# Kernel optimization log

Hardware: AMD Instinct MI355X
Metric: run time of the kernel (lower is better)

## Reference

```python
import jax, jax.numpy as jnp
import numpy as np
import math

NUM_HEADS = 16
DIM_EMB = 1024
DIM_HEAD = DIM_EMB // NUM_HEADS
BATCH = 2
SEQ = 2048


def setup_inputs() -> dict:
    key = jax.random.key(0)
    k_x, k_wq, k_bq, k_wo, k_bo = jax.random.split(key, 5)
    s_in = 1.0 / math.sqrt(DIM_EMB)
    return {
        "x": jax.random.normal(k_x, (BATCH, SEQ, DIM_EMB), dtype=jnp.float32),
        "W_qkv": jax.random.uniform(k_wq, (DIM_EMB, 3 * DIM_EMB), minval=-s_in, maxval=s_in, dtype=jnp.float32),
        "b_qkv": jax.random.uniform(k_bq, (3 * DIM_EMB,), minval=-s_in, maxval=s_in, dtype=jnp.float32),
        "W_out": jax.random.uniform(k_wo, (DIM_EMB, DIM_EMB), minval=-s_in, maxval=s_in, dtype=jnp.float32),
        "b_out": jax.random.uniform(k_bo, (DIM_EMB,), minval=-s_in, maxval=s_in, dtype=jnp.float32),
    }


def reference(x, W_qkv, b_qkv, W_out, b_out):
    B, L, E = x.shape
    H, Dh = NUM_HEADS, DIM_HEAD
    # QKV projection: (B, L, 3E)
    qkv = jnp.einsum("ble,ef->blf", x, W_qkv) + b_qkv
    # Faithful to the original's view: (B, L, 3E) -> (B, H, L, 3*Dh)
    qkv = qkv.reshape(B, H, L, 3 * Dh)
    q, k, v = jnp.split(qkv, 3, axis=-1)  # each (B, H, L, Dh)
    scale = 1.0 / math.sqrt(Dh)
    scores = jnp.einsum("bhqd,bhkd->bhqk", q, k) * scale  # (B, H, L, L)
    weights = jax.nn.softmax(scores, axis=-1)
    attn = jnp.einsum("bhqk,bhkd->bhqd", weights, v)  # (B, H, L, Dh)
    attn = attn.transpose(0, 2, 1, 3).reshape(B, L, E)
    return jnp.einsum("ble,ef->blf", attn, W_out) + b_out
```

## Files before the change

kernel.cpp:

```cpp
#include <hip/hip_runtime.h>
#include <math.h>

#define BATCH 2
#define SEQ   2048
#define EMB   1024
#define HEADS 16
#define N3E   3072
#define MROWS (BATCH*SEQ)

typedef __attribute__((ext_vector_type(8))) short  bf16x8;
typedef __attribute__((ext_vector_type(4))) float  f32x4;

__device__ __forceinline__ ushort f2bu(float f) {
    union { float f; unsigned u; } x; x.f = f;
    unsigned r = x.u + 0x7FFFu + ((x.u >> 16) & 1u);
    return (ushort)(r >> 16);
}

__global__ void cast_bf16(const float* __restrict__ in, ushort* __restrict__ out, int n4) {
    int i = blockIdx.x * blockDim.x + threadIdx.x;
    if (i < n4) {
        float4 v = ((const float4*)in)[i];
        ushort4 o;
        o.x = f2bu(v.x); o.y = f2bu(v.y); o.z = f2bu(v.z); o.w = f2bu(v.w);
        ((ushort4*)out)[i] = o;
    }
}

__global__ void transpose_cast(const float* __restrict__ W, ushort* __restrict__ Wt,
                               int K, int N) {
    __shared__ float t[32][33];
    const int bn = blockIdx.x * 32, bk = blockIdx.y * 32;
    const int tx = threadIdx.x, ty = threadIdx.y;
    #pragma unroll
    for (int j = 0; j < 4; ++j)
        t[ty + j * 8][tx] = W[(size_t)(bk + ty + j * 8) * N + bn + tx];
    __syncthreads();
    #pragma unroll
    for (int j = 0; j < 4; ++j)
        Wt[(size_t)(bn + ty + j * 8) * K + bk + tx] = f2bu(t[tx][ty + j * 8]);
}

__global__ void transpose_v(const ushort* __restrict__ qkv, ushort* __restrict__ VtG) {
    __shared__ ushort t[32][33];
    const int l0 = blockIdx.x * 32, d0 = blockIdx.y * 32, bh = blockIdx.z;
    const int rowbase = (bh >> 4) * SEQ + (bh & 15) * 128;
    const int tx = threadIdx.x, ty = threadIdx.y;
    #pragma unroll
    for (int j = 0; j < 4; ++j) {
        const int l = l0 + ty + j * 8;
        t[ty + j * 8][tx] = qkv[(size_t)(rowbase + (l >> 4)) * N3E
                                + (l & 15) * 192 + 128 + d0 + tx];
    }
    __syncthreads();
    #pragma unroll
    for (int j = 0; j < 4; ++j)
        VtG[((size_t)bh * 64 + d0 + ty + j * 8) * SEQ + l0 + tx] = t[tx][ty + j * 8];
}

template<bool OUT_BF16>
__global__ __launch_bounds__(256) void gemm_bt(const ushort* __restrict__ A,
                                               const ushort* __restrict__ Bt,
                                               const float* __restrict__ bias,
                                               void* __restrict__ Cout,
                                               int M, int N, int K)
{
    __shared__ ushort As[128][40];
    __shared__ ushort Bs[128][40];

    const int tid  = threadIdx.x;
    const int lane = tid & 63, w = tid >> 6;
    const int wr = w >> 1, wc = w & 1;
    const int l15 = lane & 15, l4 = lane >> 4;
    const int m0 = blockIdx.y * 128, n0 = blockIdx.x * 128;

    const f32x4 fzero = {0.f, 0.f, 0.f, 0.f};
    f32x4 acc[4][4];
    #pragma unroll
    for (int m = 0; m < 4; ++m)
        #pragma unroll
        for (int n = 0; n < 4; ++n) acc[m][n] = fzero;

    for (int k0 = 0; k0 < K; k0 += 32) {
        #pragma unroll
        for (int r = 0; r < 2; ++r) {
            const int i2 = tid + r * 256;
            const int row = i2 >> 2, seg = i2 & 3;
            *(bf16x8*)&As[row][seg * 8] =
                *(const bf16x8*)&A[(size_t)(m0 + row) * K + k0 + seg * 8];
            *(bf16x8*)&Bs[row][seg * 8] =
                *(const bf16x8*)&Bt[(size_t)(n0 + row) * K + k0 + seg * 8];
        }
        __syncthreads();

        bf16x8 am[4], bn[4];
        #pragma unroll
        for (int m = 0; m < 4; ++m) am[m] = *(bf16x8*)&As[wr * 64 + m * 16 + l15][l4 * 8];
        #pragma unroll
        for (int n = 0; n < 4; ++n) bn[n] = *(bf16x8*)&Bs[wc * 64 + n * 16 + l15][l4 * 8];
        #pragma unroll
        for (int m = 0; m < 4; ++m)
            #pragma unroll
            for (int n = 0; n < 4; ++n)
                acc[m][n] = __builtin_amdgcn_mfma_f32_16x16x32_bf16(am[m], bn[n], acc[m][n], 0, 0, 0);
        __syncthreads();
    }

    #pragma unroll
    for (int m = 0; m < 4; ++m)
        #pragma unroll
        for (int n = 0; n < 4; ++n)
            #pragma unroll
            for (int r = 0; r < 4; ++r) {
                const int row = m0 + wr * 64 + m * 16 + l4 * 4 + r;
                const int col = n0 + wc * 64 + n * 16 + l15;
                const float v = acc[m][n][r] + bias[col];
                if (OUT_BF16) ((ushort*)Cout)[(size_t)row * N + col] = f2bu(v);
                else          ((float*)Cout)[(size_t)row * N + col]  = v;
            }
}

__global__ __launch_bounds__(256) void mha_mfma(const ushort* __restrict__ qkv,
                                                const ushort* __restrict__ VtG,
                                                ushort* __restrict__ att)
{
    __shared__ ushort Ks [64][72];
    __shared__ ushort Vts[64][72];
    __shared__ ushort Ps [4][16][72];

    const int tid  = threadIdx.x;
    const int lane = tid & 63, w = tid >> 6;
    const int l15 = lane & 15, l4 = lane >> 4;
    const int qt = blockIdx.x, h = blockIdx.y, b = blockIdx.z;
    const size_t rowbase = (size_t)b * SEQ + (size_t)h * 128;
    const size_t vbase   = ((size_t)(b * 16 + h)) * 64 * SEQ;

    bf16x8 aq[2];
    {
        const int lq = qt * 64 + w * 16 + l15;
        const size_t base = (rowbase + (lq >> 4)) * N3E + (size_t)(lq & 15) * 192;
        aq[0] = *(const bf16x8*)&qkv[base +      l4 * 8];
        aq[1] = *(const bf16x8*)&qkv[base + 32 + l4 * 8];
    }

    const f32x4 fzero = {0.f, 0.f, 0.f, 0.f};
    float m_run[4] = {-INFINITY, -INFINITY, -INFINITY, -INFINITY};
    float l_run[4] = {0.f, 0.f, 0.f, 0.f};
    f32x4 o[4];
    #pragma unroll
    for (int f = 0; f < 4; ++f) o[f] = fzero;

    for (int jt = 0; jt < 32; ++jt) {
        __syncthreads();

        #pragma unroll
        for (int r = 0; r < 2; ++r) {
            const int i2 = tid + r * 256;
            const int row = i2 >> 3, seg = i2 & 7;
            const int kv = jt * 64 + row;
            const size_t gb = (rowbase + (kv >> 4)) * N3E + (size_t)(kv & 15) * 192;
            *(bf16x8*)&Ks[row][seg * 8]  = *(const bf16x8*)&qkv[gb + 64 + seg * 8];
            *(bf16x8*)&Vts[row][seg * 8] =
                *(const bf16x8*)&VtG[vbase + (size_t)row * SEQ + jt * 64 + seg * 8];
        }
        __syncthreads();

        f32x4 s4[4];
        #pragma unroll
        for (int f = 0; f < 4; ++f) s4[f] = fzero;
        #pragma unroll
        for (int s = 0; s < 2; ++s)
            #pragma unroll
            for (int f = 0; f < 4; ++f) {
                const bf16x8 kb = *(bf16x8*)&Ks[f * 16 + l15][s * 32 + l4 * 8];
                s4[f] = __builtin_amdgcn_mfma_f32_16x16x32_bf16(aq[s], kb, s4[f], 0, 0, 0);
            }
        #pragma unroll
        for (int f = 0; f < 4; ++f) s4[f] *= 0.125f;

        #pragma unroll
        for (int r = 0; r < 4; ++r) {
            float rm = fmaxf(fmaxf(s4[0][r], s4[1][r]), fmaxf(s4[2][r], s4[3][r]));
            rm = fmaxf(rm, __shfl_xor(rm, 1, 16));
            rm = fmaxf(rm, __shfl_xor(rm, 2, 16));
            rm = fmaxf(rm, __shfl_xor(rm, 4, 16));
            rm = fmaxf(rm, __shfl_xor(rm, 8, 16));
            const float mn   = fmaxf(m_run[r], rm);
            const float corr = __expf(m_run[r] - mn);
            float p0 = __expf(s4[0][r] - mn);
            float p1 = __expf(s4[1][r] - mn);
            float p2 = __expf(s4[2][r] - mn);
            float p3 = __expf(s4[3][r] - mn);
            float rs = p0 + p1 + p2 + p3;
            rs += __shfl_xor(rs, 1, 16);
            rs += __shfl_xor(rs, 2, 16);
            rs += __shfl_xor(rs, 4, 16);
            rs += __shfl_xor(rs, 8, 16);
            l_run[r] = l_run[r] * corr + rs;
            m_run[r] = mn;
            #pragma unroll
            for (int f = 0; f < 4; ++f) o[f][r] *= corr;
            const int qrow = l4 * 4 + r;
            Ps[w][qrow][0 * 16 + l15] = f2bu(p0);
            Ps[w][qrow][1 * 16 + l15] = f2bu(p1);
            Ps[w][qrow][2 * 16 + l15] = f2bu(p2);
            Ps[w][qrow][3 * 16 + l15] = f2bu(p3);
        }
        __syncthreads();

        #pragma unroll
        for (int s = 0; s < 2; ++s) {
            const bf16x8 pa = *(bf16x8*)&Ps[w][l15][s * 32 + l4 * 8];
            #pragma unroll
            for (int f = 0; f < 4; ++f) {
                const bf16x8 vb = *(bf16x8*)&Vts[f * 16 + l15][s * 32 + l4 * 8];
                o[f] = __builtin_amdgcn_mfma_f32_16x16x32_bf16(pa, vb, o[f], 0, 0, 0);
            }
        }
    }

    #pragma unroll
    for (int r = 0; r < 4; ++r) {
        const float inv = 1.f / l_run[r];
        const int lq = qt * 64 + w * 16 + l4 * 4 + r;
        const size_t orow = ((size_t)b * SEQ + lq) * EMB + h * 64;
        #pragma unroll
        for (int f = 0; f < 4; ++f)
            att[orow + f * 16 + l15] = f2bu(o[f][r] * inv);
    }
}

extern "C" void kernel_launch(void* const* d_in, const int* in_sizes, int n_in,
                              void* d_out, int out_size, void* d_ws, size_t ws_size,
                              hipStream_t stream)
{
    const float* x     = (const float*)d_in[0];
    const float* W_qkv = (const float*)d_in[1];
    const float* b_qkv = (const float*)d_in[2];
    const float* W_out = (const float*)d_in[3];
    const float* b_out = (const float*)d_in[4];

    ushort* xb   = (ushort*)d_ws;
    ushort* wqt  = xb   + (size_t)MROWS * EMB;
    ushort* wot  = wqt  + (size_t)N3E * EMB;
    ushort* qkvb = wot  + (size_t)EMB * EMB;
    ushort* attb = qkvb + (size_t)MROWS * N3E;
    ushort* vtg  = xb;

    cast_bf16<<<(MROWS * EMB / 4 + 255) / 256, 256, 0, stream>>>(x, xb, MROWS * EMB / 4);
    transpose_cast<<<dim3(N3E / 32, EMB / 32), dim3(32, 8), 0, stream>>>(W_qkv, wqt, EMB, N3E);
    transpose_cast<<<dim3(EMB / 32, EMB / 32), dim3(32, 8), 0, stream>>>(W_out, wot, EMB, EMB);

    gemm_bt<true><<<dim3(N3E / 128, MROWS / 128), 256, 0, stream>>>(
        xb, wqt, b_qkv, qkvb, MROWS, N3E, EMB);

    transpose_v<<<dim3(SEQ / 32, 64 / 32, BATCH * HEADS), dim3(32, 8), 0, stream>>>(qkvb, vtg);

    mha_mfma<<<dim3(SEQ / 64, HEADS, BATCH), 256, 0, stream>>>(qkvb, vtg, attb);

    gemm_bt<false><<<dim3(EMB / 128, MROWS / 128), 256, 0, stream>>>(
        attb, wot, b_out, d_out, MROWS, EMB, EMB);
}
```

Before: 283.3 us.

## Transpose attention MFMA layout, use exp2 with lazy max rescaling and packed bf16

Swaps the MFMA operand order so each lane holds one query row across its accumulator registers. Row max and sum then need only two cross-lane shuffles instead of four per row, and the running max/sum become scalars per lane. Softmax switches to exp2 with the log2e factor folded into the scale. The running-max rescale is skipped while the new max stays within a threshold of the old one. P and the output are packed to bf16 with v_cvt_pk_bf16_f32 and written as wider stores. The barrier between the P writes and the PV MMA is dropped, which is valid only because each wave reads back just its own Ps slice.

Result: faster. 233.9 us (-17.4%).

```diff
diff --git a/kernel.cpp b/kernel.cpp
--- a/kernel.cpp
+++ b/kernel.cpp
@@ -15,6 +15,20 @@
     union { float f; unsigned u; } x; x.f = f;
     unsigned r = x.u + 0x7FFFu + ((x.u >> 16) & 1u);
     return (ushort)(r >> 16);
+}
+
+__device__ __forceinline__ unsigned cvtpk_bf16(float lo, float hi) {
+    unsigned r;
+    asm("v_cvt_pk_bf16_f32 %0, %1, %2" : "=v"(r) : "v"(lo), "v"(hi));
+    return r;
+}
+
+__device__ __forceinline__ float fexp2(float x) {
+#if __has_builtin(__builtin_amdgcn_exp2f)
+    return __builtin_amdgcn_exp2f(x);
+#else
+    return exp2f(x);
+#endif
 }
 
 __global__ void cast_bf16(const float* __restrict__ in, ushort* __restrict__ out, int n4) {
@@ -144,11 +158,12 @@
     }
 
     const f32x4 fzero = {0.f, 0.f, 0.f, 0.f};
-    float m_run[4] = {-INFINITY, -INFINITY, -INFINITY, -INFINITY};
-    float l_run[4] = {0.f, 0.f, 0.f, 0.f};
+    float m_run = -INFINITY, l_run = 0.f;
     f32x4 o[4];
     #pragma unroll
     for (int f = 0; f < 4; ++f) o[f] = fzero;
+
+    const float SC = 0.125f * 1.4426950408889634f;
 
     for (int jt = 0; jt < 32; ++jt) {
         __syncthreads();
@@ -173,60 +188,71 @@
             #pragma unroll
             for (int f = 0; f < 4; ++f) {
                 const bf16x8 kb = *(bf16x8*)&Ks[f * 16 + l15][s * 32 + l4 * 8];
-                s4[f] = __builtin_amdgcn_mfma_f32_16x16x32_bf16(aq[s], kb, s4[f], 0, 0, 0);
-            }
-        #pragma unroll
-        for (int f = 0; f < 4; ++f) s4[f] *= 0.125f;
-
-        #pragma unroll
-        for (int r = 0; r < 4; ++r) {
-            float rm = fmaxf(fmaxf(s4[0][r], s4[1][r]), fmaxf(s4[2][r], s4[3][r]));
-            rm = fmaxf(rm, __shfl_xor(rm, 1, 16));
-            rm = fmaxf(rm, __shfl_xor(rm, 2, 16));
-            rm = fmaxf(rm, __shfl_xor(rm, 4, 16));
-            rm = fmaxf(rm, __shfl_xor(rm, 8, 16));
-            const float mn   = fmaxf(m_run[r], rm);
-            const float corr = __expf(m_run[r] - mn);
-            float p0 = __expf(s4[0][r] - mn);
-            float p1 = __expf(s4[1][r] - mn);
-            float p2 = __expf(s4[2][r] - mn);
-            float p3 = __expf(s4[3][r] - mn);
-            float rs = p0 + p1 + p2 + p3;
-            rs += __shfl_xor(rs, 1, 16);
-            rs += __shfl_xor(rs, 2, 16);
-            rs += __shfl_xor(rs, 4, 16);
-            rs += __shfl_xor(rs, 8, 16);
-            l_run[r] = l_run[r] * corr + rs;
-            m_run[r] = mn;
-            #pragma unroll
-            for (int f = 0; f < 4; ++f) o[f][r] *= corr;
-            const int qrow = l4 * 4 + r;
-            Ps[w][qrow][0 * 16 + l15] = f2bu(p0);
-            Ps[w][qrow][1 * 16 + l15] = f2bu(p1);
-            Ps[w][qrow][2 * 16 + l15] = f2bu(p2);
-            Ps[w][qrow][3 * 16 + l15] = f2bu(p3);
-        }
-        __syncthreads();
+                s4[f] = __builtin_amdgcn_mfma_f32_16x16x32_bf16(kb, aq[s], s4[f], 0, 0, 0);
+            }
+        #pragma unroll
+        for (int f = 0; f < 4; ++f) s4[f] *= SC;
+
+        float pmax;
+        {
+            float a0 = fmaxf(fmaxf(s4[0][0], s4[0][1]), fmaxf(s4[0][2], s4[0][3]));
+            float a1 = fmaxf(fmaxf(s4[1][0], s4[1][1]), fmaxf(s4[1][2], s4[1][3]));
+            float a2 = fmaxf(fmaxf(s4[2][0], s4[2][1]), fmaxf(s4[2][2], s4[2][3]));
+            float a3 = fmaxf(fmaxf(s4[3][0], s4[3][1]), fmaxf(s4[3][2], s4[3][3]));
+            pmax = fmaxf(fmaxf(a0, a1), fmaxf(a2, a3));
+            pmax = fmaxf(pmax, __shfl_xor(pmax, 16));
+            pmax = fmaxf(pmax, __shfl_xor(pmax, 32));
+        }
+
+        if (!__all(pmax - m_run <= 11.5f)) {
+            const float mn   = fmaxf(m_run, pmax);
+            const float corr = fexp2(m_run - mn);
+            #pragma unroll
+            for (int f = 0; f < 4; ++f) o[f] *= corr;
+            l_run *= corr;
+            m_run = mn;
+        }
+
+        float rs = 0.f;
+        #pragma unroll
+        for (int f = 0; f < 4; ++f)
+            #pragma unroll
+            for (int r = 0; r < 4; ++r) {
+                s4[f][r] = fexp2(s4[f][r] - m_run);
+                rs += s4[f][r];
+            }
+        rs += __shfl_xor(rs, 16);
+        rs += __shfl_xor(rs, 32);
+        l_run += rs;
+
+        #pragma unroll
+        for (int f = 0; f < 4; ++f) {
+            const unsigned lo = cvtpk_bf16(s4[f][0], s4[f][1]);
+            const unsigned hi = cvtpk_bf16(s4[f][2], s4[f][3]);
+            *(unsigned*)&Ps[w][l15][f * 16 + l4 * 4]     = lo;
+            *(unsigned*)&Ps[w][l15][f * 16 + l4 * 4 + 2] = hi;
+        }
 
         #pragma unroll
         for (int s = 0; s < 2; ++s) {
-            const bf16x8 pa = *(bf16x8*)&Ps[w][l15][s * 32 + l4 * 8];
+            const bf16x8 pb = *(bf16x8*)&Ps[w][l15][s * 32 + l4 * 8];
             #pragma unroll
             for (int f = 0; f < 4; ++f) {
                 const bf16x8 vb = *(bf16x8*)&Vts[f * 16 + l15][s * 32 + l4 * 8];
-                o[f] = __builtin_amdgcn_mfma_f32_16x16x32_bf16(pa, vb, o[f], 0, 0, 0);
-            }
-        }
-    }
-
-    #pragma unroll
-    for (int r = 0; r < 4; ++r) {
-        const float inv = 1.f / l_run[r];
-        const int lq = qt * 64 + w * 16 + l4 * 4 + r;
-        const size_t orow = ((size_t)b * SEQ + lq) * EMB + h * 64;
-        #pragma unroll
-        for (int f = 0; f < 4; ++f)
-            att[orow + f * 16 + l15] = f2bu(o[f][r] * inv);
+                o[f] = __builtin_amdgcn_mfma_f32_16x16x32_bf16(vb, pb, o[f], 0, 0, 0);
+            }
+        }
+    }
+
+    const float inv = 1.f / l_run;
+    const int lqo = qt * 64 + w * 16 + l15;
+    const size_t obase = ((size_t)b * SEQ + lqo) * EMB + h * 64;
+    #pragma unroll
+    for (int f = 0; f < 4; ++f) {
+        uint2 pk;
+        pk.x = cvtpk_bf16(o[f][0] * inv, o[f][1] * inv);
+        pk.y = cvtpk_bf16(o[f][2] * inv, o[f][3] * inv);
+        *(uint2*)&att[obase + f * 16 + l4 * 4] = pk;
     }
 }
 
```
